# Performance work log

Measured on AMD Instinct MI355X. Metric: run time of the kernel, lower is better.

## Reference

```python
import jax, jax.numpy as jnp
import numpy as np

EMB = 384
HEAD_DIM = 64  # emb_size / num_head = 384 / 6
B, S = 8, 2048


def setup_inputs() -> dict:
    key = jax.random.key(0)
    k1, k2, k3, k4 = jax.random.split(key, 4)
    x = jax.random.normal(k1, (B, S, EMB), dtype=jnp.float32)
    # nn.Linear(emb, head_dim, bias=False): store as [in, out] so q = x @ W
    scale = 0.02
    Wq = jax.random.normal(k2, (EMB, HEAD_DIM), dtype=jnp.float32) * scale
    Wk = jax.random.normal(k3, (EMB, HEAD_DIM), dtype=jnp.float32) * scale
    Wv = jax.random.normal(k4, (EMB, HEAD_DIM), dtype=jnp.float32) * scale
    return {"x": x, "Wq": Wq, "Wk": Wk, "Wv": Wv}


def reference(x, Wq, Wk, Wv):
    # x: [B, S, C]
    q = jnp.einsum('bsc,cd->bsd', x, Wq)  # [B,S,D]
    k = jnp.einsum('bsc,cd->bsd', x, Wk)
    v = jnp.einsum('bsc,cd->bsd', x, Wv)
    scores = jnp.einsum('bid,bjd->bij', q, k) * (HEAD_DIM ** -0.5)  # [B,S,S]
    # causal mask: positions with tril==0 (j > i) set to -inf
    causal = jnp.tril(jnp.ones((S, S), dtype=bool))  # [S,S]
    scores = jnp.where(causal[None, :, :], scores, -jnp.inf)
    # NOTE: faithful to original — softmax over dim=1 (query axis), not -1.
    attn = jax.nn.softmax(scores, axis=1)  # [B,S,S]
    out = jnp.einsum('bij,bjd->bid', attn, v)  # [B,S,D]
    return out
```

## Files before the change

### kernel.cpp

```cpp
#include <hip/hip_runtime.h>
#include <hip/hip_bf16.h>
#include <math.h>

#define B_N 8
#define S_N 2048
#define C_N 384
#define D_N 64
#define NCHUNK 16
#define NEG_BIG (-1e30f)

typedef __bf16 bf16x8 __attribute__((ext_vector_type(8)));
typedef float f32x4 __attribute__((ext_vector_type(4)));

static __device__ __forceinline__ bf16x8 ldfrag(const __bf16* p) {
  return *reinterpret_cast<const bf16x8*>(p);
}

static __device__ __forceinline__ void gload16(void* lds, const void* gsrc) {
  __builtin_amdgcn_global_load_lds(
      (const __attribute__((address_space(1))) unsigned int*)gsrc,
      (__attribute__((address_space(3))) unsigned int*)lds, 16, 0, 0);
}

__global__ __launch_bounds__(256) void w_prep(
    const float* __restrict__ Wq, const float* __restrict__ Wk,
    const float* __restrict__ Wv, __bf16* __restrict__ Wt) {
  const int idx = blockIdx.x * 256 + threadIdx.x;
  const int m = idx / (64 * C_N);
  const int r = idx % (64 * C_N);
  const int d = r / C_N;
  const int c = r % C_N;
  const float* W = (m == 0) ? Wq : (m == 1) ? Wk : Wv;
  Wt[idx] = (__bf16)W[c * 64 + d];
}

__global__ __launch_bounds__(384) void qkv_mfma(
    const float* __restrict__ x, const __bf16* __restrict__ Wt,
    __bf16* __restrict__ Q, __bf16* __restrict__ K, __bf16* __restrict__ Vt) {
  const int t = threadIdx.x;
  const int w = t >> 6, lane = t & 63, lr = lane & 15, lg = lane >> 4;
  const int mat = w >> 1, rh = w & 1;
  const int row0 = blockIdx.x * 32;
  const int ri = row0 + rh * 16 + lr;

  __shared__ __bf16 vtile[32][66];

  const float scl = (mat == 0) ? 0.125f : 1.0f;
  const float* xr = x + (size_t)ri * C_N;
  const __bf16* Wm = Wt + (size_t)mat * 64 * C_N;

  f32x4 acc[4];
#pragma unroll
  for (int nt = 0; nt < 4; ++nt) acc[nt] = {0.f, 0.f, 0.f, 0.f};

#pragma unroll 4
  for (int kk = 0; kk < C_N / 32; ++kk) {
    const float4 xa = *reinterpret_cast<const float4*>(xr + kk * 32 + lg * 8);
    const float4 xb = *reinterpret_cast<const float4*>(xr + kk * 32 + lg * 8 + 4);
    bf16x8 a;
    a[0] = (__bf16)(xa.x * scl); a[1] = (__bf16)(xa.y * scl);
    a[2] = (__bf16)(xa.z * scl); a[3] = (__bf16)(xa.w * scl);
    a[4] = (__bf16)(xb.x * scl); a[5] = (__bf16)(xb.y * scl);
    a[6] = (__bf16)(xb.z * scl); a[7] = (__bf16)(xb.w * scl);
#pragma unroll
    for (int nt = 0; nt < 4; ++nt) {
      const bf16x8 bw = ldfrag(Wm + (size_t)(nt * 16 + lr) * C_N + kk * 32 + lg * 8);
      acc[nt] = __builtin_amdgcn_mfma_f32_16x16x32_bf16(a, bw, acc[nt], 0, 0, 0);
    }
  }

  if (mat < 2) {
    __bf16* outp = (mat == 0) ? Q : K;
#pragma unroll
    for (int nt = 0; nt < 4; ++nt)
#pragma unroll
      for (int r = 0; r < 4; ++r)
        outp[(size_t)(row0 + rh * 16 + lg * 4 + r) * 64 + nt * 16 + lr] =
            (__bf16)acc[nt][r];
  } else {
#pragma unroll
    for (int nt = 0; nt < 4; ++nt)
#pragma unroll
      for (int r = 0; r < 4; ++r)
        vtile[rh * 16 + lg * 4 + r][nt * 16 + lr] = (__bf16)acc[nt][r];
  }
  __syncthreads();

  const int b = row0 >> 11, s0 = row0 & (S_N - 1);
  for (int idx = t; idx < 64 * 32; idx += 384) {
    const int d = idx >> 5, s2 = idx & 31;
    Vt[((size_t)b * D_N + d) * S_N + s0 + s2] = vtile[s2][d];
  }
}

__global__ __launch_bounds__(256) void col_part(
    const __bf16* __restrict__ Q, const __bf16* __restrict__ K,
    float* __restrict__ zP) {
  const int wg = blockIdx.x;
  const int b  = wg & 7;
  const int jb = (wg >> 3) & 31;
  const int ic = wg >> 8;
  const int j0 = jb * 64;
  const int t = threadIdx.x;
  const int iStart = max(j0, ic * (S_N / NCHUNK));
  const int iEnd = min(S_N, (ic + 1) * (S_N / NCHUNK));
  const size_t pbase = ((size_t)(b * 32 + jb) * NCHUNK + ic) * 4 * 64;

  if (iStart >= iEnd) {
    zP[pbase + t] = 0.f;
    return;
  }

  const int w = t >> 6, lane = t & 63, lr = lane & 15, lg = lane >> 4;
  const __bf16* Qb = Q + (size_t)b * S_N * 64;
  const __bf16* Kb = K + (size_t)b * S_N * 64;

  bf16x8 bk[4][2];
#pragma unroll
  for (int jt = 0; jt < 4; ++jt) {
    bk[jt][0] = ldfrag(Kb + (size_t)(j0 + jt * 16 + lr) * 64 + lg * 8);
    bk[jt][1] = ldfrag(Kb + (size_t)(j0 + jt * 16 + lr) * 64 + 32 + lg * 8);
  }

  float z4[4];
#pragma unroll
  for (int jt = 0; jt < 4; ++jt) z4[jt] = 0.f;

  bf16x8 aq0c = ldfrag(Qb + (size_t)(iStart + w * 16 + lr) * 64 + lg * 8);
  bf16x8 aq1c = ldfrag(Qb + (size_t)(iStart + w * 16 + lr) * 64 + 32 + lg * 8);

  for (int i0 = iStart; i0 < iEnd; i0 += 64) {
    const int riN = ((i0 + 64 < iEnd) ? i0 + 64 : i0) + w * 16 + lr;
    const bf16x8 aq0n = ldfrag(Qb + (size_t)riN * 64 + lg * 8);
    const bf16x8 aq1n = ldfrag(Qb + (size_t)riN * 64 + 32 + lg * 8);

    const int ibase = i0 + w * 16 + lg * 4;
    const bool diag = (i0 == j0);
#pragma unroll
    for (int jt = 0; jt < 4; ++jt) {
      f32x4 s = {0.f, 0.f, 0.f, 0.f};
      s = __builtin_amdgcn_mfma_f32_16x16x32_bf16(aq0c, bk[jt][0], s, 0, 0, 0);
      s = __builtin_amdgcn_mfma_f32_16x16x32_bf16(aq1c, bk[jt][1], s, 0, 0, 0);
      const int jg = j0 + jt * 16 + lr;
      if (diag) {
#pragma unroll
        for (int r = 0; r < 4; ++r)
          if (ibase + r < jg) s[r] = NEG_BIG;
      }
      float es = __expf(s[0]) + __expf(s[1]) + __expf(s[2]) + __expf(s[3]);
      es += __shfl_xor(es, 16);
      es += __shfl_xor(es, 32);
      z4[jt] += es;
    }
    aq0c = aq0n;
    aq1c = aq1n;
  }

  if (lg == 0) {
#pragma unroll
    for (int jt = 0; jt < 4; ++jt)
      zP[pbase + w * 64 + jt * 16 + lr] = z4[jt];
  }
}

__global__ __launch_bounds__(256) void col_reduce(
    const float* __restrict__ zP, float* __restrict__ rZ) {
  const int idx = blockIdx.x * 256 + threadIdx.x;
  const int b = idx >> 11;
  const int j = idx & (S_N - 1);
  const int jb = j >> 6, jr = j & 63;
  const size_t base = (size_t)(b * 32 + jb) * NCHUNK * 4 * 64 + jr;

  float z = 0.f;
#pragma unroll 8
  for (int p = 0; p < NCHUNK * 4; ++p) z += zP[base + (size_t)p * 64];

  rZ[idx] = 1.0f / z;
}

__global__ __launch_bounds__(1024) void attn_out(
    const __bf16* __restrict__ Q, const __bf16* __restrict__ K,
    const __bf16* __restrict__ Vt, const float* __restrict__ rZ,
    float* __restrict__ out) {
  const int wg = blockIdx.x;
  const int b  = wg & 7;
  const int ib = wg >> 3;

  const int t = threadIdx.x;
  const int w = t >> 6;
  const int s = w & 3;
  const int q = w >> 2;
  const int lane = t & 63, lr = lane & 15, lg = lane >> 4;
  const int i0 = ib * 64;

  __shared__ __align__(16) __bf16 KT[2][64][64];
  __shared__ __align__(16) __bf16 VT[2][64][64];
  __shared__ __align__(16) __bf16 P[4][16][72];

  const __bf16* Qb  = Q  + (size_t)b * S_N * 64;
  const __bf16* Kb  = K  + (size_t)b * S_N * 64;
  const __bf16* Vtb = Vt + (size_t)b * D_N * S_N;
  const float*  rZb = rZ + (size_t)b * S_N;

  const int str  = t & 511;
  const int srow = str >> 3;
  const int schk = str & 7;
  const int gchk = schk ^ (srow & 7);
  const bool isK = (t < 512);

  const int ri = i0 + s * 16 + lr;
  const bf16x8 aq0 = ldfrag(Qb + (size_t)ri * 64 + lg * 8);
  const bf16x8 aq1 = ldfrag(Qb + (size_t)ri * 64 + 32 + lg * 8);
  const int ibase = i0 + s * 16 + lg * 4;

  f32x4 o = {0.f, 0.f, 0.f, 0.f};

  if (isK) gload16(&KT[0][srow][schk * 8], Kb + (size_t)srow * 64 + gchk * 8);
  else     gload16(&VT[0][srow][schk * 8], Vtb + (size_t)srow * S_N + gchk * 8);
  __syncthreads();

  int cur = 0;
  for (int jb = 0; jb <= ib; ++jb) {
    const int j0 = jb * 64;
    if (jb + 1 <= ib) {
      const int j0n = j0 + 64;
      if (isK) gload16(&KT[cur ^ 1][srow][schk * 8],
                       Kb + (size_t)(j0n + srow) * 64 + gchk * 8);
      else     gload16(&VT[cur ^ 1][srow][schk * 8],
                       Vtb + (size_t)srow * S_N + j0n + gchk * 8);
    }

    const int krow = q * 16 + lr;
    const bf16x8 bk0 = ldfrag(&KT[cur][krow][(lg ^ (krow & 7)) * 8]);
    const bf16x8 bk1 = ldfrag(&KT[cur][krow][((4 + lg) ^ (krow & 7)) * 8]);
    f32x4 s4 = {0.f, 0.f, 0.f, 0.f};
    s4 = __builtin_amdgcn_mfma_f32_16x16x32_bf16(aq0, bk0, s4, 0, 0, 0);
    s4 = __builtin_amdgcn_mfma_f32_16x16x32_bf16(aq1, bk1, s4, 0, 0, 0);

    const int jg = j0 + q * 16 + lr;
    const float rz = rZb[jg];
#pragma unroll
    for (int r = 0; r < 4; ++r) {
      const float pv = (jg <= ibase + r) ? __expf(s4[r]) * rz : 0.f;
      P[s][lg * 4 + r][q * 16 + lr] = (__bf16)pv;
    }
    __syncthreads();

    const bf16x8 ap0 = ldfrag(&P[s][lr][lg * 8]);
    const bf16x8 ap1 = ldfrag(&P[s][lr][32 + lg * 8]);
    const int vrow = q * 16 + lr;
    const bf16x8 bv0 = ldfrag(&VT[cur][vrow][(lg ^ (vrow & 7)) * 8]);
    const bf16x8 bv1 = ldfrag(&VT[cur][vrow][((4 + lg) ^ (vrow & 7)) * 8]);
    o = __builtin_amdgcn_mfma_f32_16x16x32_bf16(ap0, bv0, o, 0, 0, 0);
    o = __builtin_amdgcn_mfma_f32_16x16x32_bf16(ap1, bv1, o, 0, 0, 0);
    __syncthreads();
    cur ^= 1;
  }

  float* ob = out + (size_t)b * S_N * D_N;
#pragma unroll
  for (int r = 0; r < 4; ++r)
    ob[(size_t)(i0 + s * 16 + lg * 4 + r) * 64 + q * 16 + lr] = o[r];
}

extern "C" void kernel_launch(void* const* d_in, const int* in_sizes, int n_in,
                              void* d_out, int out_size, void* d_ws, size_t ws_size,
                              hipStream_t stream) {
  (void)in_sizes; (void)n_in; (void)ws_size; (void)out_size;
  const float* x  = (const float*)d_in[0];
  const float* Wq = (const float*)d_in[1];
  const float* Wk = (const float*)d_in[2];
  const float* Wv = (const float*)d_in[3];
  float* out = (float*)d_out;

  __bf16* Qb = (__bf16*)d_ws;
  __bf16* Kb = Qb + (size_t)B_N * S_N * D_N;
  __bf16* Vt = Kb + (size_t)B_N * S_N * D_N;
  float* rZ = (float*)(Vt + (size_t)B_N * S_N * D_N);
  float* zP = rZ + (size_t)B_N * S_N;
  __bf16* Wt = (__bf16*)(zP + (size_t)B_N * 32 * NCHUNK * 4 * 64);

  w_prep<<<dim3(3 * 64 * C_N / 256), dim3(256), 0, stream>>>(Wq, Wk, Wv, Wt);
  qkv_mfma<<<dim3(B_N * S_N / 32), dim3(384), 0, stream>>>(x, Wt, Qb, Kb, Vt);
  col_part<<<dim3(32 * NCHUNK * B_N), dim3(256), 0, stream>>>(Qb, Kb, zP);
  col_reduce<<<dim3(B_N * S_N / 256), dim3(256), 0, stream>>>(zP, rZ);
  attn_out<<<dim3(32 * B_N), dim3(1024), 0, stream>>>(Qb, Kb, Vt, rZ, out);
}
```

Before: 90.72 us.

## Replace chunked column-sum partials and reduce kernel with single LDS-staged stats kernel

The two-stage column-normalizer computation (16-way split over query chunks writing partials, then a separate reduce kernel) is replaced by one kernel that has a 1024-thread block per (batch, 64-column block). Q tiles are double-buffered into swizzled LDS with global_load_lds, and partial sums are reduced through shared memory before writing the reciprocal. This drops a kernel launch and the partial-sum round trip through global memory. In exchange there are only 256 blocks with triangular, imbalanced work per block and a barrier on every iteration, so parallelism and load balance are lower than in the chunked version.

```diff
diff --git a/kernel.cpp b/kernel.cpp
--- a/kernel.cpp
+++ b/kernel.cpp
@@ -6,7 +6,6 @@
 #define S_N 2048
 #define C_N 384
 #define D_N 64
-#define NCHUNK 16
 #define NEG_BIG (-1e30f)
 
 typedef __bf16 bf16x8 __attribute__((ext_vector_type(8)));
@@ -93,89 +92,78 @@
   }
 }
 
-__global__ __launch_bounds__(256) void col_part(
+__global__ __launch_bounds__(1024) void col_stats(
     const __bf16* __restrict__ Q, const __bf16* __restrict__ K,
-    float* __restrict__ zP) {
+    float* __restrict__ rZ) {
   const int wg = blockIdx.x;
   const int b  = wg & 7;
-  const int jb = (wg >> 3) & 31;
-  const int ic = wg >> 8;
+  const int jb = wg >> 3;
   const int j0 = jb * 64;
+
   const int t = threadIdx.x;
-  const int iStart = max(j0, ic * (S_N / NCHUNK));
-  const int iEnd = min(S_N, (ic + 1) * (S_N / NCHUNK));
-  const size_t pbase = ((size_t)(b * 32 + jb) * NCHUNK + ic) * 4 * 64;
-
-  if (iStart >= iEnd) {
-    zP[pbase + t] = 0.f;
-    return;
-  }
-
-  const int w = t >> 6, lane = t & 63, lr = lane & 15, lg = lane >> 4;
+  const int w = t >> 6;
+  const int s = w & 3;
+  const int q = w >> 2;
+  const int lane = t & 63, lr = lane & 15, lg = lane >> 4;
+
+  __shared__ __align__(16) __bf16 QT[2][64][64];
+  __shared__ float zs[4][4][16];
+
   const __bf16* Qb = Q + (size_t)b * S_N * 64;
   const __bf16* Kb = K + (size_t)b * S_N * 64;
 
-  bf16x8 bk[4][2];
-#pragma unroll
-  for (int jt = 0; jt < 4; ++jt) {
-    bk[jt][0] = ldfrag(Kb + (size_t)(j0 + jt * 16 + lr) * 64 + lg * 8);
-    bk[jt][1] = ldfrag(Kb + (size_t)(j0 + jt * 16 + lr) * 64 + 32 + lg * 8);
-  }
-
-  float z4[4];
-#pragma unroll
-  for (int jt = 0; jt < 4; ++jt) z4[jt] = 0.f;
-
-  bf16x8 aq0c = ldfrag(Qb + (size_t)(iStart + w * 16 + lr) * 64 + lg * 8);
-  bf16x8 aq1c = ldfrag(Qb + (size_t)(iStart + w * 16 + lr) * 64 + 32 + lg * 8);
-
-  for (int i0 = iStart; i0 < iEnd; i0 += 64) {
-    const int riN = ((i0 + 64 < iEnd) ? i0 + 64 : i0) + w * 16 + lr;
-    const bf16x8 aq0n = ldfrag(Qb + (size_t)riN * 64 + lg * 8);
-    const bf16x8 aq1n = ldfrag(Qb + (size_t)riN * 64 + 32 + lg * 8);
-
-    const int ibase = i0 + w * 16 + lg * 4;
-    const bool diag = (i0 == j0);
-#pragma unroll
-    for (int jt = 0; jt < 4; ++jt) {
-      f32x4 s = {0.f, 0.f, 0.f, 0.f};
-      s = __builtin_amdgcn_mfma_f32_16x16x32_bf16(aq0c, bk[jt][0], s, 0, 0, 0);
-      s = __builtin_amdgcn_mfma_f32_16x16x32_bf16(aq1c, bk[jt][1], s, 0, 0, 0);
-      const int jg = j0 + jt * 16 + lr;
-      if (diag) {
-#pragma unroll
-        for (int r = 0; r < 4; ++r)
-          if (ibase + r < jg) s[r] = NEG_BIG;
-      }
-      float es = __expf(s[0]) + __expf(s[1]) + __expf(s[2]) + __expf(s[3]);
-      es += __shfl_xor(es, 16);
-      es += __shfl_xor(es, 32);
-      z4[jt] += es;
-    }
-    aq0c = aq0n;
-    aq1c = aq1n;
-  }
-
-  if (lg == 0) {
-#pragma unroll
-    for (int jt = 0; jt < 4; ++jt)
-      zP[pbase + w * 64 + jt * 16 + lr] = z4[jt];
-  }
-}
-
-__global__ __launch_bounds__(256) void col_reduce(
-    const float* __restrict__ zP, float* __restrict__ rZ) {
-  const int idx = blockIdx.x * 256 + threadIdx.x;
-  const int b = idx >> 11;
-  const int j = idx & (S_N - 1);
-  const int jb = j >> 6, jr = j & 63;
-  const size_t base = (size_t)(b * 32 + jb) * NCHUNK * 4 * 64 + jr;
+  const int krow = j0 + q * 16 + lr;
+  const bf16x8 bk0 = ldfrag(Kb + (size_t)krow * 64 + lg * 8);
+  const bf16x8 bk1 = ldfrag(Kb + (size_t)krow * 64 + 32 + lg * 8);
+
+  const int str  = t & 511;
+  const int srow = str >> 3;
+  const int schk = str & 7;
+  const int gchk = schk ^ (srow & 7);
+  const bool stager = (t < 512);
+
+  if (stager)
+    gload16(&QT[0][srow][schk * 8], Qb + (size_t)(j0 + srow) * 64 + gchk * 8);
+  __syncthreads();
 
   float z = 0.f;
-#pragma unroll 8
-  for (int p = 0; p < NCHUNK * 4; ++p) z += zP[base + (size_t)p * 64];
-
-  rZ[idx] = 1.0f / z;
+  int cur = 0;
+  for (int it = jb; it < 32; ++it) {
+    const int i0 = it * 64;
+    if (it + 1 < 32 && stager)
+      gload16(&QT[cur ^ 1][srow][schk * 8],
+              Qb + (size_t)(i0 + 64 + srow) * 64 + gchk * 8);
+
+    const int arow = s * 16 + lr;
+    const bf16x8 aq0 = ldfrag(&QT[cur][arow][(lg ^ (arow & 7)) * 8]);
+    const bf16x8 aq1 = ldfrag(&QT[cur][arow][((4 + lg) ^ (arow & 7)) * 8]);
+
+    f32x4 s4 = {0.f, 0.f, 0.f, 0.f};
+    s4 = __builtin_amdgcn_mfma_f32_16x16x32_bf16(aq0, bk0, s4, 0, 0, 0);
+    s4 = __builtin_amdgcn_mfma_f32_16x16x32_bf16(aq1, bk1, s4, 0, 0, 0);
+
+    const int ibase = i0 + s * 16 + lg * 4;
+    const int jg = j0 + q * 16 + lr;
+    if (it == jb) {
+#pragma unroll
+      for (int r = 0; r < 4; ++r)
+        if (ibase + r < jg) s4[r] = NEG_BIG;
+    }
+    float es = __expf(s4[0]) + __expf(s4[1]) + __expf(s4[2]) + __expf(s4[3]);
+    es += __shfl_xor(es, 16);
+    es += __shfl_xor(es, 32);
+    z += es;
+
+    __syncthreads();
+    cur ^= 1;
+  }
+
+  if (lg == 0) zs[s][q][lr] = z;
+  __syncthreads();
+  if (s == 0 && lg == 0) {
+    const float zt = zs[0][q][lr] + zs[1][q][lr] + zs[2][q][lr] + zs[3][q][lr];
+    rZ[(size_t)b * S_N + j0 + q * 16 + lr] = 1.0f / zt;
+  }
 }
 
 __global__ __launch_bounds__(1024) void attn_out(
@@ -277,12 +265,10 @@
   __bf16* Kb = Qb + (size_t)B_N * S_N * D_N;
   __bf16* Vt = Kb + (size_t)B_N * S_N * D_N;
   float* rZ = (float*)(Vt + (size_t)B_N * S_N * D_N);
-  float* zP = rZ + (size_t)B_N * S_N;
-  __bf16* Wt = (__bf16*)(zP + (size_t)B_N * 32 * NCHUNK * 4 * 64);
+  __bf16* Wt = (__bf16*)(rZ + (size_t)B_N * S_N);
 
   w_prep<<<dim3(3 * 64 * C_N / 256), dim3(256), 0, stream>>>(Wq, Wk, Wv, Wt);
   qkv_mfma<<<dim3(B_N * S_N / 32), dim3(384), 0, stream>>>(x, Wt, Qb, Kb, Vt);
-  col_part<<<dim3(32 * NCHUNK * B_N), dim3(256), 0, stream>>>(Qb, Kb, zP);
-  col_reduce<<<dim3(B_N * S_N / 256), dim3(256), 0, stream>>>(zP, rZ);
+  col_stats<<<dim3(32 * B_N), dim3(1024), 0, stream>>>(Qb, Kb, rZ);
   attn_out<<<dim3(32 * B_N), dim3(1024), 0, stream>>>(Qb, Kb, Vt, rZ, out);
 }
```

After: 83.03 us. 8.5% less time.
